# Kernel tuning notes

Measured on AMD Instinct MI355X. Metric: run time of the kernel, lower is better.

The kernel has to match this reference:

```python
import jax, jax.numpy as jnp
import numpy as np

B, T, D = 2, 4096, 512
H, K = 8, 64
F = 2048
EPS = 1e-5


def _layer_norm(x, scale, offset):
    mean = jnp.mean(x, axis=-1, keepdims=True)
    var = jnp.var(x, axis=-1, keepdims=True)
    inv = scale * jax.lax.rsqrt(var + EPS)
    return (x - mean) * inv + offset


def setup_inputs() -> dict:
    key = jax.random.key(0)
    ks = jax.random.split(key, 12)
    s = lambda fan_in: (2.0 / fan_in) ** 0.5  # VarianceScaling(2.0) std
    inputs = jax.random.normal(ks[0], (B, T, D), jnp.float32)
    return {
        "inputs": inputs,
        "ln1_scale": jnp.ones((D,), jnp.float32),
        "ln1_offset": jnp.zeros((D,), jnp.float32),
        "wq": jax.random.normal(ks[1], (D, H * K), jnp.float32) * s(D),
        "bq": jnp.zeros((H * K,), jnp.float32),
        "wk": jax.random.normal(ks[2], (D, H * K), jnp.float32) * s(D),
        "bk": jnp.zeros((H * K,), jnp.float32),
        "wv": jax.random.normal(ks[3], (D, H * K), jnp.float32) * s(D),
        "bv": jnp.zeros((H * K,), jnp.float32),
        "wo": jax.random.normal(ks[4], (H * K, D), jnp.float32) * s(H * K),
        "bo": jnp.zeros((D,), jnp.float32),
        "ln2_scale": jnp.ones((D,), jnp.float32),
        "ln2_offset": jnp.zeros((D,), jnp.float32),
        "w1": jax.random.normal(ks[5], (D, F), jnp.float32) * (1.0 / D) ** 0.5,
        "b1": jnp.zeros((F,), jnp.float32),
        "w2": jax.random.normal(ks[6], (F, D), jnp.float32) * (1.0 / F) ** 0.5,
        "b2": jnp.zeros((D,), jnp.float32),
    }


def reference(inputs, ln1_scale, ln1_offset, wq, bq, wk, bk, wv, bv, wo, bo,
              ln2_scale, ln2_offset, w1, b1, w2, b2):
    # --- pre-attention LayerNorm ---
    x1 = _layer_norm(inputs, ln1_scale, ln1_offset)
    # --- multi-head attention (eval mode, no mask) ---
    q = (x1 @ wq + bq).reshape(B, T, H, K)
    k = (x1 @ wk + bk).reshape(B, T, H, K)
    v = (x1 @ wv + bv).reshape(B, T, H, K)
    logits = jnp.einsum('bthd,bshd->bhts', q, k) / jnp.sqrt(jnp.asarray(K, q.dtype))
    attn = jax.nn.softmax(logits, axis=-1)
    ctx = jnp.einsum('bhts,bshd->bthd', attn, v).reshape(B, T, H * K)
    attn_out = ctx @ wo + bo
    # --- residual ---
    x = inputs + attn_out
    # --- pre-FFN LayerNorm + GELU FFN ---
    y = _layer_norm(x, ln2_scale, ln2_offset)
    ff = jax.nn.gelu(y @ w1 + b1) @ w2 + b2
    return x + ff
```

## Files before the change

### kernel.cpp

```cpp
#include <hip/hip_runtime.h>
#include <hip/hip_bf16.h>

typedef __attribute__((ext_vector_type(4))) float f32x4;
typedef __attribute__((ext_vector_type(8))) short short8;
typedef __attribute__((ext_vector_type(2))) unsigned u32x2;

#define DEV __device__ __forceinline__

DEV short f2bf(float f) {
    union { float f; unsigned u; } a; a.f = f;
    unsigned r = a.u + 0x7fffu + ((a.u >> 16) & 1u);
    return (short)(r >> 16);
}

DEV float bf2f(short s) {
    union { unsigned u; float f; } a;
    a.u = ((unsigned)(unsigned short)s) << 16;
    return a.f;
}

DEV unsigned cvt_pk_bf16(float a, float b) {
    unsigned r;
    asm("v_cvt_pk_bf16_f32 %0, %1, %2" : "=v"(r) : "v"(a), "v"(b));
    return r;
}

DEV float exp2_fast(float x) { return __builtin_amdgcn_exp2f(x); }

DEV void gload16(const short* g, short* l) {
    __builtin_amdgcn_global_load_lds(
        (__attribute__((address_space(1))) void*)g,
        (__attribute__((address_space(3))) void*)l, 16, 0, 0);
}

DEV float gelu_f(float x) {
    float u = 0.7978845608028654f * (x + 0.044715f * x * x * x);
    float e = __expf(2.0f * u);
    float t = 1.0f - 2.0f / (e + 1.0f);
    return 0.5f * x * (1.0f + t);
}

__global__ __launch_bounds__(256) void ln_kernel(const float* __restrict__ x,
                                                 const float* __restrict__ scale,
                                                 const float* __restrict__ offset,
                                                 short* __restrict__ out) {
    const int wid = threadIdx.x >> 6, lane = threadIdx.x & 63;
    const long row = (long)blockIdx.x * 4 + wid;
    const float* xr = x + row * 512;
    f32x4 v0 = *(const f32x4*)&xr[lane * 8];
    f32x4 v1 = *(const f32x4*)&xr[lane * 8 + 4];
    float s = 0.f, sq = 0.f;
#pragma unroll
    for (int i = 0; i < 4; i++) {
        s += v0[i] + v1[i];
        sq += v0[i] * v0[i] + v1[i] * v1[i];
    }
#pragma unroll
    for (int m = 1; m < 64; m <<= 1) { s += __shfl_xor(s, m); sq += __shfl_xor(sq, m); }
    float mean = s * (1.0f / 512.0f);
    float var = sq * (1.0f / 512.0f) - mean * mean;
    float inv = rsqrtf(var + 1e-5f);
    f32x4 sc0 = *(const f32x4*)&scale[lane * 8];
    f32x4 sc1 = *(const f32x4*)&scale[lane * 8 + 4];
    f32x4 of0 = *(const f32x4*)&offset[lane * 8];
    f32x4 of1 = *(const f32x4*)&offset[lane * 8 + 4];
    short8 o;
#pragma unroll
    for (int i = 0; i < 4; i++) {
        o[i]     = f2bf((v0[i] - mean) * inv * sc0[i] + of0[i]);
        o[4 + i] = f2bf((v1[i] - mean) * inv * sc1[i] + of1[i]);
    }
    *(short8*)&out[row * 512 + lane * 8] = o;
}

__global__ __launch_bounds__(256) void prep_kernel(const float* __restrict__ wq,
                                                   const float* __restrict__ wk,
                                                   const float* __restrict__ wv,
                                                   const float* __restrict__ wo,
                                                   const float* __restrict__ w1,
                                                   const float* __restrict__ w2,
                                                   const float* __restrict__ bq,
                                                   const float* __restrict__ bk,
                                                   const float* __restrict__ bv,
                                                   short* __restrict__ wqkvt,
                                                   short* __restrict__ wot,
                                                   short* __restrict__ w1t,
                                                   short* __restrict__ w2t,
                                                   float* __restrict__ bqkv) {
    const int bid = blockIdx.x;
    if (bid == 768) {
        for (int i = threadIdx.x; i < 512; i += 256) {
            bqkv[i] = bq[i]; bqkv[512 + i] = bk[i]; bqkv[1024 + i] = bv[i];
        }
        return;
    }
    const float* src; short* dst; int Kd, N, kt, nt;
    if (bid < 256) {
        Kd = 512; N = 512;
        const int which = bid >> 6, local = bid & 63;
        kt = local & 7; nt = local >> 3;
        if (which == 0)      { src = wq; dst = wqkvt; }
        else if (which == 1) { src = wk; dst = wqkvt + 512 * 512; }
        else if (which == 2) { src = wv; dst = wqkvt + 2 * 512 * 512; }
        else                 { src = wo; dst = wot; }
    } else if (bid < 512) {
        src = w1; dst = w1t; Kd = 512; N = 2048;
        const int local = bid - 256; kt = local & 7; nt = local >> 3;
    } else {
        src = w2; dst = w2t; Kd = 2048; N = 512;
        const int local = bid - 512; kt = local & 31; nt = local >> 5;
    }
    __shared__ float tile[64][65];
    const int k0 = kt * 64, n0 = nt * 64;
    const int tid = threadIdx.x;
#pragma unroll
    for (int ld = 0; ld < 4; ld++) {
        int li = ld * 1024 + tid * 4;
        int r = li >> 6, c = li & 63;
        f32x4 tv = *(const f32x4*)&src[(long)(k0 + r) * N + n0 + c];
        tile[r][c] = tv[0]; tile[r][c + 1] = tv[1];
        tile[r][c + 2] = tv[2]; tile[r][c + 3] = tv[3];
    }
    __syncthreads();
#pragma unroll
    for (int st = 0; st < 2; st++) {
        int li = st * 2048 + tid * 8;
        int r = li >> 6, c = li & 63;
        short8 o;
#pragma unroll
        for (int i = 0; i < 8; i++) o[i] = f2bf(tile[c + i][r]);
        *(short8*)&dst[(long)(n0 + r) * Kd + k0 + c] = o;
    }
}

template <int BM, bool GELU_ACT, bool OUT_BF16, bool RESID>
__global__ __launch_bounds__(256) void gemm_bt(const short* __restrict__ A,
                                               const short* __restrict__ Bt,
                                               const float* __restrict__ bias,
                                               const float* __restrict__ resid,
                                               void* __restrict__ Cout,
                                               int M, int N, int Kd) {
    constexpr int NR = (BM == 128) ? 4 : 2;
    constexpr int LA = BM / 32;
    __shared__ short Asm[BM][64];
    __shared__ short Bsm[128][64];
    const int tid = threadIdx.x;
    const int wid = tid >> 6, lane = tid & 63;
    const int lr = lane & 15, lg = lane >> 4;
    const int row0 = blockIdx.x * BM, col0 = blockIdx.y * 128;
    const int wm = (BM == 128) ? (wid >> 1) * 64 : 0;
    const int wn = (BM == 128) ? (wid & 1) * 64 : wid * 32;

    f32x4 acc[4][NR];
#pragma unroll
    for (int m = 0; m < 4; m++)
#pragma unroll
        for (int n = 0; n < NR; n++)
#pragma unroll
            for (int j = 0; j < 4; j++) acc[m][n][j] = 0.f;

    const int swr = (lr & 7) << 3;

    for (int k0 = 0; k0 < Kd; k0 += 64) {
#pragma unroll
        for (int ld = 0; ld < LA; ld++) {
            int off = ld * 2048 + tid * 8;
            int r = off >> 6, c = off & 63;
            int sc = c ^ ((r & 7) << 3);
            gload16(&A[(long)(row0 + r) * Kd + k0 + sc], &Asm[0][0] + off);
        }
#pragma unroll
        for (int ld = 0; ld < 4; ld++) {
            int off = ld * 2048 + tid * 8;
            int r = off >> 6, c = off & 63;
            int sc = c ^ ((r & 7) << 3);
            gload16(&Bt[(long)(col0 + r) * Kd + k0 + sc], &Bsm[0][0] + off);
        }
        __syncthreads();
#pragma unroll
        for (int kk = 0; kk < 64; kk += 32) {
            short8 af[4], bf[NR];
#pragma unroll
            for (int m = 0; m < 4; m++) af[m] = *(const short8*)&Asm[wm + m * 16 + lr][(kk + lg * 8) ^ swr];
#pragma unroll
            for (int n = 0; n < NR; n++) bf[n] = *(const short8*)&Bsm[wn + n * 16 + lr][(kk + lg * 8) ^ swr];
#pragma unroll
            for (int m = 0; m < 4; m++)
#pragma unroll
                for (int n = 0; n < NR; n++)
                    acc[m][n] = __builtin_amdgcn_mfma_f32_16x16x32_bf16(af[m], bf[n], acc[m][n], 0, 0, 0);
        }
        __syncthreads();
    }

#pragma unroll
    for (int m = 0; m < 4; m++) {
#pragma unroll
        for (int n = 0; n < NR; n++) {
#pragma unroll
            for (int j = 0; j < 4; j++) {
                int r = row0 + wm + m * 16 + lg * 4 + j;
                int c = col0 + wn + n * 16 + lr;
                float v = acc[m][n][j] + bias[c];
                if constexpr (GELU_ACT) v = gelu_f(v);
                if constexpr (RESID) v += resid[(long)r * N + c];
                if constexpr (OUT_BF16) ((short*)Cout)[(long)r * N + c] = f2bf(v);
                else                    ((float*)Cout)[(long)r * N + c] = v;
            }
        }
    }
}

__global__ __launch_bounds__(256) void attn_kernel(const short* __restrict__ q,
                                                   const short* __restrict__ k,
                                                   const short* __restrict__ v,
                                                   float* __restrict__ opart,
                                                   float* __restrict__ mpart,
                                                   float* __restrict__ lpart) {
    __shared__ short Ksm[128][64];
    __shared__ short Vsm[64][136];
    __shared__ short Psm[4][16][136];
    const int tid = threadIdx.x, wid = tid >> 6, lane = tid & 63;
    const int lr = lane & 15, lg = lane >> 4;
    const int bh = blockIdx.y, b = bh >> 3, h = bh & 7;
    const int t0 = blockIdx.x * 128;
    const int split = blockIdx.z;
    const int s_begin = split * 2048, s_end = s_begin + 2048;
    const long base = (long)b * 4096 * 1536 + h * 64;

    short8 qf[2][2];
#pragma unroll
    for (int rg = 0; rg < 2; rg++) {
        const long qoff = base + (long)(t0 + wid * 32 + rg * 16 + lr) * 1536 + lg * 8;
        short8 q0 = *(const short8*)&q[qoff];
        short8 q1 = *(const short8*)&q[qoff + 32];
#pragma unroll
        for (int i = 0; i < 8; i++) {
            qf[rg][0][i] = f2bf(bf2f(q0[i]) * 0.18033688f);
            qf[rg][1][i] = f2bf(bf2f(q1[i]) * 0.18033688f);
        }
    }

    f32x4 o[2][4];
    float mrow[2], lrow[2];
#pragma unroll
    for (int rg = 0; rg < 2; rg++) {
        mrow[rg] = -1e30f; lrow[rg] = 0.f;
#pragma unroll
        for (int n = 0; n < 4; n++)
#pragma unroll
            for (int j = 0; j < 4; j++) o[rg][n][j] = 0.f;
    }

    const int skey = tid >> 3, sd = (tid & 7) * 8, sm = tid & 7;
    short8 kreg[4], vreg[4];
#pragma unroll
    for (int p = 0; p < 4; p++) {
        long off = base + (long)(s_begin + p * 32 + skey) * 1536 + sd;
        kreg[p] = *(const short8*)&k[off];
        vreg[p] = *(const short8*)&v[off];
    }

    for (int s0 = s_begin; s0 < s_end; s0 += 128) {
        __syncthreads();
#pragma unroll
        for (int p = 0; p < 4; p++) {
            int key = p * 32 + skey;
            *(short8*)&Ksm[key][sd ^ ((key & 7) << 3)] = kreg[p];
            int kc = key ^ (sm << 3);
#pragma unroll
            for (int i = 0; i < 8; i++) Vsm[sd + i][kc] = vreg[p][i];
        }
        __syncthreads();
        if (s0 + 128 < s_end) {
#pragma unroll
            for (int p = 0; p < 4; p++) {
                long off = base + (long)(s0 + 128 + p * 32 + skey) * 1536 + sd;
                kreg[p] = *(const short8*)&k[off];
                vreg[p] = *(const short8*)&v[off];
            }
        }

        const int ksw = (lr & 7) << 3;
#pragma unroll
        for (int rg = 0; rg < 2; rg++) {
            f32x4 s[8];
#pragma unroll
            for (int c = 0; c < 8; c++) { s[c][0] = 0.f; s[c][1] = 0.f; s[c][2] = 0.f; s[c][3] = 0.f; }
            __builtin_amdgcn_s_setprio(1);
#pragma unroll
            for (int c = 0; c < 8; c++) {
                const int krow = c * 16 + lr;
                short8 kf0 = *(const short8*)&Ksm[krow][(lg * 8) ^ ksw];
                short8 kf1 = *(const short8*)&Ksm[krow][(32 + lg * 8) ^ ksw];
                s[c] = __builtin_amdgcn_mfma_f32_16x16x32_bf16(kf0, qf[rg][0], s[c], 0, 0, 0);
                s[c] = __builtin_amdgcn_mfma_f32_16x16x32_bf16(kf1, qf[rg][1], s[c], 0, 0, 0);
            }
            __builtin_amdgcn_s_setprio(0);

            f32x4 m4 = s[0];
#pragma unroll
            for (int c = 1; c < 8; c++)
#pragma unroll
                for (int j = 0; j < 4; j++) m4[j] = fmaxf(m4[j], s[c][j]);
            float mx = fmaxf(fmaxf(m4[0], m4[1]), fmaxf(m4[2], m4[3]));
            mx = fmaxf(mx, __shfl_xor(mx, 16));
            mx = fmaxf(mx, __shfl_xor(mx, 32));
            float mn = mrow[rg];
            if (!__all(mx <= mn + 8.0f)) {
                mn = fmaxf(mrow[rg], mx);
                float alpha = exp2_fast(mrow[rg] - mn);
                mrow[rg] = mn;
                lrow[rg] *= alpha;
#pragma unroll
                for (int j = 0; j < 4; j++) {
                    float aj = __shfl(alpha, lg * 4 + j);
#pragma unroll
                    for (int n = 0; n < 4; n++) o[rg][n][j] *= aj;
                }
            }
            f32x4 sum4 = {0.f, 0.f, 0.f, 0.f};
#pragma unroll
            for (int c = 0; c < 8; c++)
#pragma unroll
                for (int j = 0; j < 4; j++) {
                    float e = exp2_fast(s[c][j] - mn);
                    s[c][j] = e;
                    sum4[j] += e;
                }
            float rs = (sum4[0] + sum4[1]) + (sum4[2] + sum4[3]);
            rs += __shfl_xor(rs, 16);
            rs += __shfl_xor(rs, 32);
            lrow[rg] += rs;

#pragma unroll
            for (int c = 0; c < 8; c++) {
                u32x2 w;
                w[0] = cvt_pk_bf16(s[c][0], s[c][1]);
                w[1] = cvt_pk_bf16(s[c][2], s[c][3]);
                *(u32x2*)&Psm[wid][lr][c * 16 + lg * 4] = w;
            }
            short8 pa[4];
#pragma unroll
            for (int kk = 0; kk < 4; kk++) pa[kk] = *(const short8*)&Psm[wid][lr][kk * 32 + lg * 8];

            __builtin_amdgcn_s_setprio(1);
#pragma unroll
            for (int n = 0; n < 4; n++) {
                const int vrow = n * 16 + lr;
                const int vsw = ((vrow >> 3) & 7) << 3;
#pragma unroll
                for (int kk = 0; kk < 4; kk++) {
                    short8 vf = *(const short8*)&Vsm[vrow][(kk * 32 + lg * 8) ^ vsw];
                    o[rg][n] = __builtin_amdgcn_mfma_f32_16x16x32_bf16(pa[kk], vf, o[rg][n], 0, 0, 0);
                }
            }
            __builtin_amdgcn_s_setprio(0);
        }
    }

    const long rowbase = (long)b * 4096 + t0 + wid * 32;
    const long ob = ((long)split * 8192 + rowbase) * 512 + h * 64;
#pragma unroll
    for (int rg = 0; rg < 2; rg++)
#pragma unroll
        for (int j = 0; j < 4; j++)
#pragma unroll
            for (int n = 0; n < 4; n++)
                opart[ob + (long)(rg * 16 + lg * 4 + j) * 512 + n * 16 + lr] = o[rg][n][j];
    if (lane < 16) {
#pragma unroll
        for (int rg = 0; rg < 2; rg++) {
            long idx = ((long)split * 8192 + rowbase + rg * 16 + lr) * 8 + h;
            mpart[idx] = mrow[rg];
            lpart[idx] = lrow[rg];
        }
    }
}

__global__ __launch_bounds__(256) void attn_merge(const float* __restrict__ op,
                                                  const float* __restrict__ mp,
                                                  const float* __restrict__ lp,
                                                  short* __restrict__ ctx) {
    const int wid = threadIdx.x >> 6, lane = threadIdx.x & 63;
    const long row = (long)blockIdx.x * 4 + wid;
    const int c0 = lane * 8, h = c0 >> 6;
    float m0 = mp[row * 8 + h], m1 = mp[(8192 + row) * 8 + h];
    float l0 = lp[row * 8 + h], l1 = lp[(8192 + row) * 8 + h];
    float M = fmaxf(m0, m1);
    float w0 = exp2_fast(m0 - M), w1 = exp2_fast(m1 - M);
    float inv = 1.0f / (w0 * l0 + w1 * l1);
    w0 *= inv; w1 *= inv;
    f32x4 a0 = *(const f32x4*)&op[row * 512 + c0];
    f32x4 a1 = *(const f32x4*)&op[row * 512 + c0 + 4];
    f32x4 b0 = *(const f32x4*)&op[(8192 + row) * 512 + c0];
    f32x4 b1 = *(const f32x4*)&op[(8192 + row) * 512 + c0 + 4];
    short8 o;
#pragma unroll
    for (int i = 0; i < 4; i++) {
        o[i]     = f2bf(w0 * a0[i] + w1 * b0[i]);
        o[4 + i] = f2bf(w0 * a1[i] + w1 * b1[i]);
    }
    *(short8*)&ctx[row * 512 + c0] = o;
}

extern "C" void kernel_launch(void* const* d_in, const int* in_sizes, int n_in,
                              void* d_out, int out_size, void* d_ws, size_t ws_size,
                              hipStream_t stream) {
    (void)in_sizes; (void)n_in; (void)out_size; (void)ws_size;
    const float* inputs = (const float*)d_in[0];
    const float* ln1_s  = (const float*)d_in[1];
    const float* ln1_o  = (const float*)d_in[2];
    const float* wq     = (const float*)d_in[3];
    const float* bq     = (const float*)d_in[4];
    const float* wk     = (const float*)d_in[5];
    const float* bk     = (const float*)d_in[6];
    const float* wv     = (const float*)d_in[7];
    const float* bv     = (const float*)d_in[8];
    const float* wo     = (const float*)d_in[9];
    const float* bo     = (const float*)d_in[10];
    const float* ln2_s  = (const float*)d_in[11];
    const float* ln2_o  = (const float*)d_in[12];
    const float* w1     = (const float*)d_in[13];
    const float* b1     = (const float*)d_in[14];
    const float* w2     = (const float*)d_in[15];
    const float* b2     = (const float*)d_in[16];
    float* out = (float*)d_out;

    char* p = (char*)d_ws;
    auto alloc = [&](size_t bytes) { void* r = (void*)p; p += (bytes + 255) & ~(size_t)255; return r; };
    short* x1    = (short*)alloc((size_t)8192 * 512 * 2);
    short* qkvb  = (short*)alloc((size_t)8192 * 1536 * 2);
    short* ctxb  = (short*)alloc((size_t)8192 * 512 * 2);
    short* yb    = (short*)alloc((size_t)8192 * 512 * 2);
    short* hb    = (short*)alloc((size_t)8192 * 2048 * 2);
    short* wqkvt = (short*)alloc((size_t)1536 * 512 * 2);
    short* wot   = (short*)alloc((size_t)512 * 512 * 2);
    short* w1t   = (short*)alloc((size_t)2048 * 512 * 2);
    short* w2t   = (short*)alloc((size_t)512 * 2048 * 2);
    float* bqkv  = (float*)alloc((size_t)1536 * 4);
    float* opart = (float*)alloc((size_t)2 * 8192 * 512 * 4);
    float* mpart = (float*)alloc((size_t)2 * 8192 * 8 * 4);
    float* lpart = (float*)alloc((size_t)2 * 8192 * 8 * 4);

    dim3 blk(256);
    prep_kernel<<<769, blk, 0, stream>>>(wq, wk, wv, wo, w1, w2, bq, bk, bv,
                                         wqkvt, wot, w1t, w2t, bqkv);
    ln_kernel<<<2048, blk, 0, stream>>>(inputs, ln1_s, ln1_o, x1);
    gemm_bt<128, false, true, false><<<dim3(64, 12), blk, 0, stream>>>(x1, wqkvt, bqkv, nullptr, qkvb, 8192, 1536, 512);
    attn_kernel<<<dim3(32, 16, 2), blk, 0, stream>>>(qkvb, qkvb + 512, qkvb + 1024, opart, mpart, lpart);
    attn_merge<<<2048, blk, 0, stream>>>(opart, mpart, lpart, ctxb);
    gemm_bt<64, false, false, true><<<dim3(128, 4), blk, 0, stream>>>(ctxb, wot, bo, inputs, out, 8192, 512, 512);
    ln_kernel<<<2048, blk, 0, stream>>>(out, ln2_s, ln2_o, yb);
    gemm_bt<128, true, true, false><<<dim3(64, 16), blk, 0, stream>>>(yb, w1t, b1, nullptr, hb, 8192, 2048, 512);
    gemm_bt<64, false, false, true><<<dim3(128, 4), blk, 0, stream>>>(hb, w2t, b2, out, out, 8192, 512, 2048);
}
```

Before: 350.5 us.

## Rewrite attention with 32x32x16 MFMA, register softmax, and async K loads

The flash-attention kernel switches from 16x16x32 to 32x32x16 bf16 MFMAs. With S computed transposed (keys by queries), each lane owns one query row, so the row max and sum need only one cross-lane shuffle. P is repacked in registers with v_permlane32_swap instead of a round trip through LDS, and the Psm buffer is removed. K tiles are now double-buffered and loaded straight into LDS with global_load_lds, while V still goes through registers with a transposing store. This aims to cut LDS traffic, shuffle overhead and sync stalls, at the cost of larger accumulator register use and a more complex layout that is easy to get wrong.

```diff
diff --git a/kernel.cpp b/kernel.cpp
--- a/kernel.cpp
+++ b/kernel.cpp
@@ -2,8 +2,8 @@
 #include <hip/hip_bf16.h>
 
 typedef __attribute__((ext_vector_type(4))) float f32x4;
+typedef __attribute__((ext_vector_type(16))) float f32x16;
 typedef __attribute__((ext_vector_type(8))) short short8;
-typedef __attribute__((ext_vector_type(2))) unsigned u32x2;
 
 #define DEV __device__ __forceinline__
 
@@ -23,6 +23,10 @@
     unsigned r;
     asm("v_cvt_pk_bf16_f32 %0, %1, %2" : "=v"(r) : "v"(a), "v"(b));
     return r;
+}
+
+DEV void permlane32_swap(unsigned& a, unsigned& b) {
+    asm("v_permlane32_swap_b32 %0, %1" : "+v"(a), "+v"(b));
 }
 
 DEV float exp2_fast(float x) { return __builtin_amdgcn_exp2f(x); }
@@ -217,143 +221,137 @@
                                                    float* __restrict__ opart,
                                                    float* __restrict__ mpart,
                                                    float* __restrict__ lpart) {
-    __shared__ short Ksm[128][64];
+    __shared__ short Ksm[2][128][64];
     __shared__ short Vsm[64][136];
-    __shared__ short Psm[4][16][136];
     const int tid = threadIdx.x, wid = tid >> 6, lane = tid & 63;
-    const int lr = lane & 15, lg = lane >> 4;
+    const int lo = lane & 31, hi = lane >> 5;
     const int bh = blockIdx.y, b = bh >> 3, h = bh & 7;
     const int t0 = blockIdx.x * 128;
     const int split = blockIdx.z;
-    const int s_begin = split * 2048, s_end = s_begin + 2048;
+    const int s_begin = split * 2048;
     const long base = (long)b * 4096 * 1536 + h * 64;
 
-    short8 qf[2][2];
-#pragma unroll
-    for (int rg = 0; rg < 2; rg++) {
-        const long qoff = base + (long)(t0 + wid * 32 + rg * 16 + lr) * 1536 + lg * 8;
-        short8 q0 = *(const short8*)&q[qoff];
-        short8 q1 = *(const short8*)&q[qoff + 32];
-#pragma unroll
-        for (int i = 0; i < 8; i++) {
-            qf[rg][0][i] = f2bf(bf2f(q0[i]) * 0.18033688f);
-            qf[rg][1][i] = f2bf(bf2f(q1[i]) * 0.18033688f);
-        }
-    }
-
-    f32x4 o[2][4];
-    float mrow[2], lrow[2];
-#pragma unroll
-    for (int rg = 0; rg < 2; rg++) {
-        mrow[rg] = -1e30f; lrow[rg] = 0.f;
-#pragma unroll
-        for (int n = 0; n < 4; n++)
-#pragma unroll
-            for (int j = 0; j < 4; j++) o[rg][n][j] = 0.f;
-    }
+    short8 qb[4];
+    {
+        const long qrow = base + (long)(t0 + wid * 32 + lo) * 1536;
+#pragma unroll
+        for (int s = 0; s < 4; s++) {
+            short8 t = *(const short8*)&q[qrow + s * 16 + hi * 8];
+#pragma unroll
+            for (int i = 0; i < 8; i++) t[i] = f2bf(bf2f(t[i]) * 0.18033688f);
+            qb[s] = t;
+        }
+    }
+
+    f32x16 o0, o1;
+#pragma unroll
+    for (int i = 0; i < 16; i++) { o0[i] = 0.f; o1[i] = 0.f; }
+    float mn = -1e30f, lsum = 0.f;
 
     const int skey = tid >> 3, sd = (tid & 7) * 8, sm = tid & 7;
-    short8 kreg[4], vreg[4];
-#pragma unroll
-    for (int p = 0; p < 4; p++) {
-        long off = base + (long)(s_begin + p * 32 + skey) * 1536 + sd;
-        kreg[p] = *(const short8*)&k[off];
-        vreg[p] = *(const short8*)&v[off];
-    }
-
-    for (int s0 = s_begin; s0 < s_end; s0 += 128) {
-        __syncthreads();
+    short8 vreg[4];
+#pragma unroll
+    for (int it = 0; it < 4; it++) {
+        int off = it * 2048 + tid * 8;
+        int r = off >> 6, cc = off & 63;
+        int sc = cc ^ ((r & 7) << 3);
+        gload16(&k[base + (long)(s_begin + r) * 1536 + sc], &Ksm[0][0][0] + off);
+    }
+#pragma unroll
+    for (int p = 0; p < 4; p++)
+        vreg[p] = *(const short8*)&v[base + (long)(s_begin + p * 32 + skey) * 1536 + sd];
+
+    for (int tile = 0; tile < 16; tile++) {
+        const int cur = tile & 1;
+        __builtin_amdgcn_s_barrier();
 #pragma unroll
         for (int p = 0; p < 4; p++) {
             int key = p * 32 + skey;
-            *(short8*)&Ksm[key][sd ^ ((key & 7) << 3)] = kreg[p];
             int kc = key ^ (sm << 3);
 #pragma unroll
             for (int i = 0; i < 8; i++) Vsm[sd + i][kc] = vreg[p][i];
         }
-        __syncthreads();
-        if (s0 + 128 < s_end) {
-#pragma unroll
-            for (int p = 0; p < 4; p++) {
-                long off = base + (long)(s0 + 128 + p * 32 + skey) * 1536 + sd;
-                kreg[p] = *(const short8*)&k[off];
-                vreg[p] = *(const short8*)&v[off];
-            }
-        }
-
-        const int ksw = (lr & 7) << 3;
-#pragma unroll
-        for (int rg = 0; rg < 2; rg++) {
-            f32x4 s[8];
-#pragma unroll
-            for (int c = 0; c < 8; c++) { s[c][0] = 0.f; s[c][1] = 0.f; s[c][2] = 0.f; s[c][3] = 0.f; }
+        if (tile + 1 < 16) {
+            const int s0n = s_begin + (tile + 1) * 128;
+#pragma unroll
+            for (int it = 0; it < 4; it++) {
+                int off = it * 2048 + tid * 8;
+                int r = off >> 6, cc = off & 63;
+                int sc = cc ^ ((r & 7) << 3);
+                gload16(&k[base + (long)(s0n + r) * 1536 + sc], &Ksm[cur ^ 1][0][0] + off);
+            }
+#pragma unroll
+            for (int p = 0; p < 4; p++)
+                vreg[p] = *(const short8*)&v[base + (long)(s0n + p * 32 + skey) * 1536 + sd];
+        }
+        asm volatile("s_waitcnt lgkmcnt(0)" ::: "memory");
+        __builtin_amdgcn_sched_barrier(0);
+        __builtin_amdgcn_s_barrier();
+
+#pragma unroll
+        for (int c = 0; c < 4; c++) {
+            const int key = c * 32 + lo;
+            const int kx = (key & 7) << 3;
+            const short* kp = &Ksm[cur][key][0];
+            f32x16 sa;
+#pragma unroll
+            for (int i = 0; i < 16; i++) sa[i] = 0.f;
             __builtin_amdgcn_s_setprio(1);
 #pragma unroll
-            for (int c = 0; c < 8; c++) {
-                const int krow = c * 16 + lr;
-                short8 kf0 = *(const short8*)&Ksm[krow][(lg * 8) ^ ksw];
-                short8 kf1 = *(const short8*)&Ksm[krow][(32 + lg * 8) ^ ksw];
-                s[c] = __builtin_amdgcn_mfma_f32_16x16x32_bf16(kf0, qf[rg][0], s[c], 0, 0, 0);
-                s[c] = __builtin_amdgcn_mfma_f32_16x16x32_bf16(kf1, qf[rg][1], s[c], 0, 0, 0);
+            for (int s = 0; s < 4; s++) {
+                short8 ka = *(const short8*)&kp[(s * 16 + hi * 8) ^ kx];
+                sa = __builtin_amdgcn_mfma_f32_32x32x16_bf16(ka, qb[s], sa, 0, 0, 0);
             }
             __builtin_amdgcn_s_setprio(0);
 
-            f32x4 m4 = s[0];
-#pragma unroll
-            for (int c = 1; c < 8; c++)
-#pragma unroll
-                for (int j = 0; j < 4; j++) m4[j] = fmaxf(m4[j], s[c][j]);
-            float mx = fmaxf(fmaxf(m4[0], m4[1]), fmaxf(m4[2], m4[3]));
-            mx = fmaxf(mx, __shfl_xor(mx, 16));
-            mx = fmaxf(mx, __shfl_xor(mx, 32));
-            float mn = mrow[rg];
-            if (!__all(mx <= mn + 8.0f)) {
-                mn = fmaxf(mrow[rg], mx);
-                float alpha = exp2_fast(mrow[rg] - mn);
-                mrow[rg] = mn;
-                lrow[rg] *= alpha;
-#pragma unroll
-                for (int j = 0; j < 4; j++) {
-                    float aj = __shfl(alpha, lg * 4 + j);
-#pragma unroll
-                    for (int n = 0; n < 4; n++) o[rg][n][j] *= aj;
+            float cm = fmaxf(sa[0], sa[1]);
+#pragma unroll
+            for (int i = 2; i < 16; i++) cm = fmaxf(cm, sa[i]);
+            cm = fmaxf(cm, __shfl_xor(cm, 32));
+            if (!__all(cm <= mn + 8.0f)) {
+                float nm = fmaxf(mn, cm);
+                float alpha = exp2_fast(mn - nm);
+                mn = nm; lsum *= alpha;
+#pragma unroll
+                for (int r = 0; r < 16; r++) {
+                    int qr = (r & 3) + 8 * (r >> 2) + 4 * hi;
+                    float ar = __shfl(alpha, qr);
+                    o0[r] *= ar; o1[r] *= ar;
                 }
             }
-            f32x4 sum4 = {0.f, 0.f, 0.f, 0.f};
-#pragma unroll
-            for (int c = 0; c < 8; c++)
-#pragma unroll
-                for (int j = 0; j < 4; j++) {
-                    float e = exp2_fast(s[c][j] - mn);
-                    s[c][j] = e;
-                    sum4[j] += e;
-                }
-            float rs = (sum4[0] + sum4[1]) + (sum4[2] + sum4[3]);
-            rs += __shfl_xor(rs, 16);
-            rs += __shfl_xor(rs, 32);
-            lrow[rg] += rs;
-
-#pragma unroll
-            for (int c = 0; c < 8; c++) {
-                u32x2 w;
-                w[0] = cvt_pk_bf16(s[c][0], s[c][1]);
-                w[1] = cvt_pk_bf16(s[c][2], s[c][3]);
-                *(u32x2*)&Psm[wid][lr][c * 16 + lg * 4] = w;
-            }
-            short8 pa[4];
-#pragma unroll
-            for (int kk = 0; kk < 4; kk++) pa[kk] = *(const short8*)&Psm[wid][lr][kk * 32 + lg * 8];
-
+            float ls = 0.f;
+#pragma unroll
+            for (int r = 0; r < 16; r++) {
+                float e = exp2_fast(sa[r] - mn);
+                sa[r] = e; ls += e;
+            }
+            lsum += ls;
+
+            unsigned w0 = cvt_pk_bf16(sa[0], sa[1]),   w1 = cvt_pk_bf16(sa[2], sa[3]);
+            unsigned w2 = cvt_pk_bf16(sa[4], sa[5]),   w3 = cvt_pk_bf16(sa[6], sa[7]);
+            unsigned w4 = cvt_pk_bf16(sa[8], sa[9]),   w5 = cvt_pk_bf16(sa[10], sa[11]);
+            unsigned w6 = cvt_pk_bf16(sa[12], sa[13]), w7 = cvt_pk_bf16(sa[14], sa[15]);
+            permlane32_swap(w0, w2);
+            permlane32_swap(w1, w3);
+            permlane32_swap(w4, w6);
+            permlane32_swap(w5, w7);
+            union { unsigned u[4]; short8 s8; } pa0, pa1;
+            pa0.u[0] = w0; pa0.u[1] = w1; pa0.u[2] = w2; pa0.u[3] = w3;
+            pa1.u[0] = w4; pa1.u[1] = w5; pa1.u[2] = w6; pa1.u[3] = w7;
+
+            const int vc = c * 32 + hi * 8;
+            const int d0 = lo, d1 = 32 + lo;
+            const int vs0 = ((d0 >> 3) & 7) << 3, vs1 = ((d1 >> 3) & 7) << 3;
             __builtin_amdgcn_s_setprio(1);
-#pragma unroll
-            for (int n = 0; n < 4; n++) {
-                const int vrow = n * 16 + lr;
-                const int vsw = ((vrow >> 3) & 7) << 3;
-#pragma unroll
-                for (int kk = 0; kk < 4; kk++) {
-                    short8 vf = *(const short8*)&Vsm[vrow][(kk * 32 + lg * 8) ^ vsw];
-                    o[rg][n] = __builtin_amdgcn_mfma_f32_16x16x32_bf16(pa[kk], vf, o[rg][n], 0, 0, 0);
-                }
+            {
+                short8 vb00 = *(const short8*)&Vsm[d0][vc ^ vs0];
+                short8 vb01 = *(const short8*)&Vsm[d0][(vc + 16) ^ vs0];
+                o0 = __builtin_amdgcn_mfma_f32_32x32x16_bf16(pa0.s8, vb00, o0, 0, 0, 0);
+                o0 = __builtin_amdgcn_mfma_f32_32x32x16_bf16(pa1.s8, vb01, o0, 0, 0, 0);
+                short8 vb10 = *(const short8*)&Vsm[d1][vc ^ vs1];
+                short8 vb11 = *(const short8*)&Vsm[d1][(vc + 16) ^ vs1];
+                o1 = __builtin_amdgcn_mfma_f32_32x32x16_bf16(pa0.s8, vb10, o1, 0, 0, 0);
+                o1 = __builtin_amdgcn_mfma_f32_32x32x16_bf16(pa1.s8, vb11, o1, 0, 0, 0);
             }
             __builtin_amdgcn_s_setprio(0);
         }
@@ -362,19 +360,16 @@
     const long rowbase = (long)b * 4096 + t0 + wid * 32;
     const long ob = ((long)split * 8192 + rowbase) * 512 + h * 64;
 #pragma unroll
-    for (int rg = 0; rg < 2; rg++)
-#pragma unroll
-        for (int j = 0; j < 4; j++)
-#pragma unroll
-            for (int n = 0; n < 4; n++)
-                opart[ob + (long)(rg * 16 + lg * 4 + j) * 512 + n * 16 + lr] = o[rg][n][j];
-    if (lane < 16) {
-#pragma unroll
-        for (int rg = 0; rg < 2; rg++) {
-            long idx = ((long)split * 8192 + rowbase + rg * 16 + lr) * 8 + h;
-            mpart[idx] = mrow[rg];
-            lpart[idx] = lrow[rg];
-        }
+    for (int r = 0; r < 16; r++) {
+        int qr = (r & 3) + 8 * (r >> 2) + 4 * hi;
+        opart[ob + (long)qr * 512 + lo]      = o0[r];
+        opart[ob + (long)qr * 512 + 32 + lo] = o1[r];
+    }
+    lsum += __shfl_xor(lsum, 32);
+    if (lane < 32) {
+        long idx = ((long)split * 8192 + rowbase + lo) * 8 + h;
+        mpart[idx] = mn;
+        lpart[idx] = lsum;
     }
 }
 
```

Measured after the change: 332.8 us. -5.0%, faster.
